# Kernel optimization log

Hardware: AMD Instinct MI355X
Metric: run time of the kernel (lower is better)

## Reference

```python
import jax, jax.numpy as jnp
import numpy as np

PARTIAL_DATA_THRESHOLD = 0.1  # threshold on squared NN distance (ChamferDistance returns squared dists)


def setup_inputs() -> dict:
    key = jax.random.key(0)
    k1, k2 = jax.random.split(key)
    scan_vertices = jax.random.normal(k1, (50000, 3), dtype=jnp.float32)      # N x 3
    template_vertices = jax.random.normal(k2, (6890, 3), dtype=jnp.float32)   # M x 3
    return {"scan_vertices": scan_vertices, "template_vertices": template_vertices}


def reference(scan_vertices, template_vertices):
    # Directional (template -> scan) Chamfer: for each template point, squared
    # distance to nearest scan point; then sum distances below threshold.
    # d2[m, n] = |t_m|^2 + |s_n|^2 - 2 t_m . s_n
    t_sq = jnp.sum(template_vertices * template_vertices, axis=-1)            # [M]
    s_sq = jnp.sum(scan_vertices * scan_vertices, axis=-1)                    # [N]
    cross = jnp.einsum('md,nd->mn', template_vertices, scan_vertices)         # [M, N]
    d2 = t_sq[:, None] + s_sq[None, :] - 2.0 * cross                          # [M, N]
    template2scan = jnp.min(d2, axis=1)                                       # [M]
    mask = template2scan < PARTIAL_DATA_THRESHOLD
    return jnp.sum(jnp.where(mask, template2scan, 0.0))
```

## Files before the change

### kernel.cpp

```cpp
#include <hip/hip_runtime.h>
#include <hip/hip_bf16.h>

#define BLK 256
#define WPB 4
#define TB 12
#define TSPLITS 18
#define SA 11
#define SSPLITS 144
#define FRTOT 1584
#define NSLOT (FRTOT * 32)
#define MFR 216
#define MPAD (MFR * 32)
#define THRESH 0.1f
#define KEY_MAX 0xFFFFFFFFu
#define ONE_BF ((unsigned short)0x3F80)

typedef __attribute__((ext_vector_type(8))) short short8;
typedef __attribute__((ext_vector_type(16))) float floatx16;

__device__ __forceinline__ unsigned short f2bf(float x) {
    unsigned u = __float_as_uint(x);
    unsigned r = u + 0x7FFFu + ((u >> 16) & 1u);
    return (unsigned short)(r >> 16);
}
__device__ __forceinline__ float bf2f(unsigned short h) {
    return __uint_as_float(((unsigned)h) << 16);
}

__device__ __forceinline__ unsigned f2key(float f) {
    unsigned b = __float_as_uint(f);
    return (b & 0x80000000u) ? ~b : (b | 0x80000000u);
}
__device__ __forceinline__ float key2f(unsigned k) {
    return __uint_as_float((k & 0x80000000u) ? (k & 0x7FFFFFFFu) : ~k);
}

__global__ __launch_bounds__(BLK) void pdl_prep(const float* __restrict__ scan,
                                                const float* __restrict__ tmpl,
                                                uint4* __restrict__ afrag,
                                                uint4* __restrict__ bfrag,
                                                unsigned* __restrict__ gmin,
                                                float* __restrict__ out,
                                                int N, int M) {
    const int n = blockIdx.x * BLK + threadIdx.x;
    if (n == 0) out[0] = 0.0f;

    if (n < MPAD) {
        gmin[n] = KEY_MAX;
        unsigned short q[16];
        if (n < M) {
            const float x = tmpl[3 * n + 0], y = tmpl[3 * n + 1], z = tmpl[3 * n + 2];
            const float t2 = fmaf(x, x, fmaf(y, y, z * z));
            const unsigned short xh = f2bf(x); const unsigned short xl = f2bf(x - bf2f(xh));
            const unsigned short yh = f2bf(y); const unsigned short yl = f2bf(y - bf2f(yh));
            const unsigned short zh = f2bf(z); const unsigned short zl = f2bf(z - bf2f(zh));
            const unsigned short wh = f2bf(t2); const unsigned short wl = f2bf(t2 - bf2f(wh));
            q[0] = xh; q[1] = xh; q[2] = xl; q[3] = xl;
            q[4] = yh; q[5] = yh; q[6] = yl; q[7] = yl;
            q[8] = zh; q[9] = zh; q[10] = zl; q[11] = zl;
            q[12] = wh; q[13] = wl;
            q[14] = ONE_BF; q[15] = ONE_BF;
        } else {
#pragma unroll
            for (int i = 0; i < 16; ++i) q[i] = 0;
            q[14] = ONE_BF; q[15] = ONE_BF;
        }
        const int g = n >> 5, c = n & 31;
        uint4 lo, hi;
        lo.x = (unsigned)q[0] | ((unsigned)q[1] << 16);
        lo.y = (unsigned)q[2] | ((unsigned)q[3] << 16);
        lo.z = (unsigned)q[4] | ((unsigned)q[5] << 16);
        lo.w = (unsigned)q[6] | ((unsigned)q[7] << 16);
        hi.x = (unsigned)q[8] | ((unsigned)q[9] << 16);
        hi.y = (unsigned)q[10] | ((unsigned)q[11] << 16);
        hi.z = (unsigned)q[12] | ((unsigned)q[13] << 16);
        hi.w = (unsigned)q[14] | ((unsigned)q[15] << 16);
        bfrag[(size_t)g * 64 + c] = lo;
        bfrag[(size_t)g * 64 + 32 + c] = hi;
    }

    if (n >= NSLOT) return;

    unsigned short k[16];
    if (n < N) {
        const float x = scan[3 * n + 0], y = scan[3 * n + 1], z = scan[3 * n + 2];
        const float s2 = fmaf(x, x, fmaf(y, y, z * z));
        const float cx = -2.0f * x, cy = -2.0f * y, cz = -2.0f * z;
        const unsigned short xh = f2bf(cx); const unsigned short xl = f2bf(cx - bf2f(xh));
        const unsigned short yh = f2bf(cy); const unsigned short yl = f2bf(cy - bf2f(yh));
        const unsigned short zh = f2bf(cz); const unsigned short zl = f2bf(cz - bf2f(zh));
        const unsigned short wh = f2bf(s2); const unsigned short wl = f2bf(s2 - bf2f(wh));
        k[0] = xh; k[1] = xl; k[2] = xh; k[3] = xl;
        k[4] = yh; k[5] = yl; k[6] = yh; k[7] = yl;
        k[8] = zh; k[9] = zl; k[10] = zh; k[11] = zl;
        k[12] = ONE_BF; k[13] = ONE_BF;
        k[14] = wh; k[15] = wl;
    } else {
#pragma unroll
        for (int i = 0; i < 16; ++i) k[i] = 0;
        k[12] = ONE_BF; k[13] = ONE_BF;
        k[14] = f2bf(1e30f); k[15] = 0;
    }

    const int g = n >> 5, c = n & 31;
    uint4 lo, hi;
    lo.x = (unsigned)k[0] | ((unsigned)k[1] << 16);
    lo.y = (unsigned)k[2] | ((unsigned)k[3] << 16);
    lo.z = (unsigned)k[4] | ((unsigned)k[5] << 16);
    lo.w = (unsigned)k[6] | ((unsigned)k[7] << 16);
    hi.x = (unsigned)k[8] | ((unsigned)k[9] << 16);
    hi.y = (unsigned)k[10] | ((unsigned)k[11] << 16);
    hi.z = (unsigned)k[12] | ((unsigned)k[13] << 16);
    hi.w = (unsigned)k[14] | ((unsigned)k[15] << 16);
    afrag[(size_t)g * 64 + c] = lo;
    afrag[(size_t)g * 64 + 32 + c] = hi;
}

__global__ __launch_bounds__(BLK, 3) void pdl_main(const uint4* __restrict__ afrag,
                                                   const uint4* __restrict__ bfrag,
                                                   unsigned* __restrict__ gmin) {
    const int tid = threadIdx.x;
    const int wave = tid >> 6, lane = tid & 63;
    const int tsplit = blockIdx.x;
    const int ssplit = blockIdx.y * WPB + wave;

    __shared__ unsigned lmin[TB * 32];
#pragma unroll 2
    for (int i = tid; i < TB * 32; i += BLK) lmin[i] = KEY_MAX;

    union U { uint4 u; short8 s; };

    const uint4* bb = bfrag + (size_t)(tsplit * TB) * 64 + lane;
    U B[TB];
#pragma unroll
    for (int j = 0; j < TB; ++j) B[j].u = bb[(size_t)j * 64];

    float mn[TB];
#pragma unroll
    for (int j = 0; j < TB; ++j) mn[j] = 3e30f;

    floatx16 zacc;
#pragma unroll
    for (int r = 0; r < 16; ++r) zacc[r] = 0.0f;

    __syncthreads();

    const uint4* ab = afrag + (size_t)(ssplit * SA) * 64 + lane;
    uint4 p = ab[0];
#pragma unroll 1
    for (int f = 0; f < SA; ++f) {
        U a; a.u = p;
        p = ab[(size_t)(f + 1) * 64];
#pragma unroll
        for (int j = 0; j < TB; ++j) {
            const floatx16 d =
                __builtin_amdgcn_mfma_f32_32x32x16_bf16(a.s, B[j].s, zacc, 0, 0, 0);
            const float t0 = fminf(fminf(d[0], d[1]), d[2]);
            const float t1 = fminf(fminf(d[3], d[4]), d[5]);
            const float t2 = fminf(fminf(d[6], d[7]), d[8]);
            const float t3 = fminf(fminf(d[9], d[10]), d[11]);
            const float t4 = fminf(fminf(d[12], d[13]), d[14]);
            const float u0 = fminf(fminf(t0, t1), t2);
            const float u1 = fminf(fminf(t3, t4), d[15]);
            mn[j] = fminf(fminf(u0, u1), mn[j]);
        }
    }

#pragma unroll
    for (int j = 0; j < TB; ++j) {
        const float o = __shfl_xor(mn[j], 32, 64);
        const float v = fminf(mn[j], o);
        if (lane < 32) atomicMin(&lmin[j * 32 + lane], f2key(v));
    }
    __syncthreads();

    const int mbase = tsplit * (TB * 32);
#pragma unroll 2
    for (int i = tid; i < TB * 32; i += BLK) atomicMin(&gmin[mbase + i], lmin[i]);
}

__global__ __launch_bounds__(BLK) void pdl_final(const unsigned* __restrict__ gmin,
                                                 float* __restrict__ out, int M) {
    const int m = blockIdx.x * BLK + threadIdx.x;
    float s = 0.0f;
    if (m < M) {
        const float v = key2f(gmin[m]);
        if (v < THRESH) s = v;
    }
#pragma unroll
    for (int off = 32; off > 0; off >>= 1) s += __shfl_down(s, off, 64);

    __shared__ float ls[BLK / 64];
    const int lane = threadIdx.x & 63;
    const int w = threadIdx.x >> 6;
    if (lane == 0) ls[w] = s;
    __syncthreads();
    if (threadIdx.x == 0) {
        float t = 0.0f;
#pragma unroll
        for (int i = 0; i < BLK / 64; ++i) t += ls[i];
        atomicAdd(out, t);
    }
}

extern "C" void kernel_launch(void* const* d_in, const int* in_sizes, int n_in,
                              void* d_out, int out_size, void* d_ws, size_t ws_size,
                              hipStream_t stream) {
    const float* scan = (const float*)d_in[0];
    const float* tmpl = (const float*)d_in[1];
    float* out = (float*)d_out;

    const int N = in_sizes[0] / 3;
    const int M = in_sizes[1] / 3;

    unsigned* gmin = (unsigned*)d_ws;
    uint4* afrag = (uint4*)((char*)d_ws + 65536);
    uint4* bfrag = (uint4*)((char*)d_ws + 65536 + (size_t)(FRTOT + 2) * 1024);

    pdl_prep<<<(NSLOT + BLK - 1) / BLK, BLK, 0, stream>>>(scan, tmpl, afrag, bfrag,
                                                          gmin, out, N, M);

    dim3 grid(TSPLITS, SSPLITS / WPB);
    pdl_main<<<grid, BLK, 0, stream>>>(afrag, bfrag, gmin);

    pdl_final<<<(M + BLK - 1) / BLK, BLK, 0, stream>>>(gmin, out, M);
}
```

Before: 73.03 us.

## Fuse fragment preparation into main kernel and replace global atomics with partial buffers

Removes the separate prep kernel: the main kernel now loads raw scan and template points and builds the split-bf16 MFMA fragments in registers, prefetching the next scan point each iteration. Global atomicMin into a shared min array is replaced by per-scan-group partial minima written to workspace, which the final kernel reduces over 36 groups. This saves a launch and the fragment round-trip through memory, at the cost of extra conversion ALU work inside the MFMA loop and a larger final reduction.

```diff
diff --git a/kernel.cpp b/kernel.cpp
--- a/kernel.cpp
+++ b/kernel.cpp
@@ -6,14 +6,11 @@
 #define TB 12
 #define TSPLITS 18
 #define SA 11
-#define SSPLITS 144
-#define FRTOT 1584
-#define NSLOT (FRTOT * 32)
-#define MFR 216
-#define MPAD (MFR * 32)
+#define SGROUPS 36
+#define COLS (TSPLITS * TB * 32)
 #define THRESH 0.1f
 #define KEY_MAX 0xFFFFFFFFu
-#define ONE_BF ((unsigned short)0x3F80)
+#define ONE2 0x3F803F80u
 
 typedef __attribute__((ext_vector_type(8))) short short8;
 typedef __attribute__((ext_vector_type(16))) float floatx16;
@@ -26,6 +23,11 @@
 __device__ __forceinline__ float bf2f(unsigned short h) {
     return __uint_as_float(((unsigned)h) << 16);
 }
+__device__ __forceinline__ unsigned packsplit(float v) {
+    const unsigned short h = f2bf(v);
+    const unsigned short l = f2bf(v - bf2f(h));
+    return (unsigned)h | ((unsigned)l << 16);
+}
 
 __device__ __forceinline__ unsigned f2key(float f) {
     unsigned b = __float_as_uint(f);
@@ -35,94 +37,52 @@
     return __uint_as_float((k & 0x80000000u) ? (k & 0x7FFFFFFFu) : ~k);
 }
 
-__global__ __launch_bounds__(BLK) void pdl_prep(const float* __restrict__ scan,
-                                                const float* __restrict__ tmpl,
-                                                uint4* __restrict__ afrag,
-                                                uint4* __restrict__ bfrag,
-                                                unsigned* __restrict__ gmin,
-                                                float* __restrict__ out,
-                                                int N, int M) {
-    const int n = blockIdx.x * BLK + threadIdx.x;
-    if (n == 0) out[0] = 0.0f;
-
-    if (n < MPAD) {
-        gmin[n] = KEY_MAX;
-        unsigned short q[16];
-        if (n < M) {
-            const float x = tmpl[3 * n + 0], y = tmpl[3 * n + 1], z = tmpl[3 * n + 2];
-            const float t2 = fmaf(x, x, fmaf(y, y, z * z));
-            const unsigned short xh = f2bf(x); const unsigned short xl = f2bf(x - bf2f(xh));
-            const unsigned short yh = f2bf(y); const unsigned short yl = f2bf(y - bf2f(yh));
-            const unsigned short zh = f2bf(z); const unsigned short zl = f2bf(z - bf2f(zh));
-            const unsigned short wh = f2bf(t2); const unsigned short wl = f2bf(t2 - bf2f(wh));
-            q[0] = xh; q[1] = xh; q[2] = xl; q[3] = xl;
-            q[4] = yh; q[5] = yh; q[6] = yl; q[7] = yl;
-            q[8] = zh; q[9] = zh; q[10] = zl; q[11] = zl;
-            q[12] = wh; q[13] = wl;
-            q[14] = ONE_BF; q[15] = ONE_BF;
-        } else {
-#pragma unroll
-            for (int i = 0; i < 16; ++i) q[i] = 0;
-            q[14] = ONE_BF; q[15] = ONE_BF;
-        }
-        const int g = n >> 5, c = n & 31;
-        uint4 lo, hi;
-        lo.x = (unsigned)q[0] | ((unsigned)q[1] << 16);
-        lo.y = (unsigned)q[2] | ((unsigned)q[3] << 16);
-        lo.z = (unsigned)q[4] | ((unsigned)q[5] << 16);
-        lo.w = (unsigned)q[6] | ((unsigned)q[7] << 16);
-        hi.x = (unsigned)q[8] | ((unsigned)q[9] << 16);
-        hi.y = (unsigned)q[10] | ((unsigned)q[11] << 16);
-        hi.z = (unsigned)q[12] | ((unsigned)q[13] << 16);
-        hi.w = (unsigned)q[14] | ((unsigned)q[15] << 16);
-        bfrag[(size_t)g * 64 + c] = lo;
-        bfrag[(size_t)g * 64 + 32 + c] = hi;
-    }
-
-    if (n >= NSLOT) return;
-
-    unsigned short k[16];
-    if (n < N) {
-        const float x = scan[3 * n + 0], y = scan[3 * n + 1], z = scan[3 * n + 2];
-        const float s2 = fmaf(x, x, fmaf(y, y, z * z));
-        const float cx = -2.0f * x, cy = -2.0f * y, cz = -2.0f * z;
-        const unsigned short xh = f2bf(cx); const unsigned short xl = f2bf(cx - bf2f(xh));
-        const unsigned short yh = f2bf(cy); const unsigned short yl = f2bf(cy - bf2f(yh));
-        const unsigned short zh = f2bf(cz); const unsigned short zl = f2bf(cz - bf2f(zh));
-        const unsigned short wh = f2bf(s2); const unsigned short wl = f2bf(s2 - bf2f(wh));
-        k[0] = xh; k[1] = xl; k[2] = xh; k[3] = xl;
-        k[4] = yh; k[5] = yl; k[6] = yh; k[7] = yl;
-        k[8] = zh; k[9] = zl; k[10] = zh; k[11] = zl;
-        k[12] = ONE_BF; k[13] = ONE_BF;
-        k[14] = wh; k[15] = wl;
-    } else {
-#pragma unroll
-        for (int i = 0; i < 16; ++i) k[i] = 0;
-        k[12] = ONE_BF; k[13] = ONE_BF;
-        k[14] = f2bf(1e30f); k[15] = 0;
-    }
-
-    const int g = n >> 5, c = n & 31;
-    uint4 lo, hi;
-    lo.x = (unsigned)k[0] | ((unsigned)k[1] << 16);
-    lo.y = (unsigned)k[2] | ((unsigned)k[3] << 16);
-    lo.z = (unsigned)k[4] | ((unsigned)k[5] << 16);
-    lo.w = (unsigned)k[6] | ((unsigned)k[7] << 16);
-    hi.x = (unsigned)k[8] | ((unsigned)k[9] << 16);
-    hi.y = (unsigned)k[10] | ((unsigned)k[11] << 16);
-    hi.z = (unsigned)k[12] | ((unsigned)k[13] << 16);
-    hi.w = (unsigned)k[14] | ((unsigned)k[15] << 16);
-    afrag[(size_t)g * 64 + c] = lo;
-    afrag[(size_t)g * 64 + 32 + c] = hi;
+__device__ __forceinline__ uint4 build_scan_frag(float x, float y, float z, bool hi) {
+    const float s2 = fmaf(x, x, fmaf(y, y, z * z));
+    const float c0 = -2.0f * (hi ? z : x);
+    const float c1 = hi ? s2 : (-2.0f * y);
+    const unsigned w01 = packsplit(c0);
+    const unsigned w23 = packsplit(c1);
+    uint4 u;
+    u.x = w01; u.y = w01;
+    u.z = hi ? ONE2 : w23;
+    u.w = w23;
+    return u;
 }
 
-__global__ __launch_bounds__(BLK, 3) void pdl_main(const uint4* __restrict__ afrag,
-                                                   const uint4* __restrict__ bfrag,
-                                                   unsigned* __restrict__ gmin) {
+__device__ __forceinline__ uint4 build_tmpl_frag(const float* __restrict__ tmpl,
+                                                 int c, bool hi) {
+    const float x = tmpl[3 * c + 0], y = tmpl[3 * c + 1], z = tmpl[3 * c + 2];
+    const float t2 = fmaf(x, x, fmaf(y, y, z * z));
+    const float a0 = hi ? z : x;
+    const float a1 = hi ? t2 : y;
+    const unsigned short h0 = f2bf(a0);
+    const unsigned short l0 = f2bf(a0 - bf2f(h0));
+    const unsigned short h1 = f2bf(a1);
+    const unsigned short l1 = f2bf(a1 - bf2f(h1));
+    uint4 u;
+    u.x = (unsigned)h0 | ((unsigned)h0 << 16);
+    u.y = (unsigned)l0 | ((unsigned)l0 << 16);
+    u.z = hi ? ((unsigned)h1 | ((unsigned)l1 << 16))
+             : ((unsigned)h1 | ((unsigned)h1 << 16));
+    u.w = hi ? ONE2
+             : ((unsigned)l1 | ((unsigned)l1 << 16));
+    return u;
+}
+
+__global__ __launch_bounds__(BLK, 3) void pdl_main(const float* __restrict__ scan,
+                                                   const float* __restrict__ tmpl,
+                                                   unsigned* __restrict__ partial,
+                                                   float* __restrict__ out,
+                                                   int N, int M) {
     const int tid = threadIdx.x;
     const int wave = tid >> 6, lane = tid & 63;
+    const bool hi = (lane >= 32);
     const int tsplit = blockIdx.x;
-    const int ssplit = blockIdx.y * WPB + wave;
+    const int sgroup = blockIdx.y;
+    const int ssplit = sgroup * WPB + wave;
+
+    if (tsplit == 0 && sgroup == 0 && tid == 0) out[0] = 0.0f;
 
     __shared__ unsigned lmin[TB * 32];
 #pragma unroll 2
@@ -130,10 +90,14 @@
 
     union U { uint4 u; short8 s; };
 
-    const uint4* bb = bfrag + (size_t)(tsplit * TB) * 64 + lane;
     U B[TB];
+    const int cbase = tsplit * (TB * 32) + (lane & 31);
 #pragma unroll
-    for (int j = 0; j < TB; ++j) B[j].u = bb[(size_t)j * 64];
+    for (int j = 0; j < TB; ++j) {
+        int c = cbase + j * 32;
+        if (c > M - 1) c = M - 1;
+        B[j].u = build_tmpl_frag(tmpl, c, hi);
+    }
 
     float mn[TB];
 #pragma unroll
@@ -143,14 +107,16 @@
 #pragma unroll
     for (int r = 0; r < 16; ++r) zacc[r] = 0.0f;
 
-    __syncthreads();
-
-    const uint4* ab = afrag + (size_t)(ssplit * SA) * 64 + lane;
-    uint4 p = ab[0];
+    const int nbase = ssplit * (SA * 32) + (lane & 31);
+    int n0 = nbase; if (n0 > N - 1) n0 = N - 1;
+    float x = scan[3 * n0 + 0], y = scan[3 * n0 + 1], z = scan[3 * n0 + 2];
 #pragma unroll 1
     for (int f = 0; f < SA; ++f) {
-        U a; a.u = p;
-        p = ab[(size_t)(f + 1) * 64];
+        int n1 = nbase + (f + 1) * 32; if (n1 > N - 1) n1 = N - 1;
+        const float nx = scan[3 * n1 + 0];
+        const float ny = scan[3 * n1 + 1];
+        const float nz = scan[3 * n1 + 2];
+        U a; a.u = build_scan_frag(x, y, z, hi);
 #pragma unroll
         for (int j = 0; j < TB; ++j) {
             const floatx16 d =
@@ -164,7 +130,10 @@
             const float u1 = fminf(fminf(t3, t4), d[15]);
             mn[j] = fminf(fminf(u0, u1), mn[j]);
         }
+        x = nx; y = ny; z = nz;
     }
+
+    __syncthreads();
 
 #pragma unroll
     for (int j = 0; j < TB; ++j) {
@@ -174,17 +143,21 @@
     }
     __syncthreads();
 
-    const int mbase = tsplit * (TB * 32);
+    const size_t base = (size_t)sgroup * COLS + (size_t)tsplit * (TB * 32);
 #pragma unroll 2
-    for (int i = tid; i < TB * 32; i += BLK) atomicMin(&gmin[mbase + i], lmin[i]);
+    for (int i = tid; i < TB * 32; i += BLK) partial[base + i] = lmin[i];
 }
 
-__global__ __launch_bounds__(BLK) void pdl_final(const unsigned* __restrict__ gmin,
+__global__ __launch_bounds__(BLK) void pdl_final(const unsigned* __restrict__ partial,
                                                  float* __restrict__ out, int M) {
     const int m = blockIdx.x * BLK + threadIdx.x;
     float s = 0.0f;
     if (m < M) {
-        const float v = key2f(gmin[m]);
+        unsigned k = KEY_MAX;
+#pragma unroll 4
+        for (int g = 0; g < SGROUPS; ++g)
+            k = min(k, partial[(size_t)g * COLS + m]);
+        const float v = key2f(k);
         if (v < THRESH) s = v;
     }
 #pragma unroll
@@ -213,15 +186,10 @@
     const int N = in_sizes[0] / 3;
     const int M = in_sizes[1] / 3;
 
-    unsigned* gmin = (unsigned*)d_ws;
-    uint4* afrag = (uint4*)((char*)d_ws + 65536);
-    uint4* bfrag = (uint4*)((char*)d_ws + 65536 + (size_t)(FRTOT + 2) * 1024);
+    unsigned* partial = (unsigned*)d_ws;
 
-    pdl_prep<<<(NSLOT + BLK - 1) / BLK, BLK, 0, stream>>>(scan, tmpl, afrag, bfrag,
-                                                          gmin, out, N, M);
+    dim3 grid(TSPLITS, SGROUPS);
+    pdl_main<<<grid, BLK, 0, stream>>>(scan, tmpl, partial, out, N, M);
 
-    dim3 grid(TSPLITS, SSPLITS / WPB);
-    pdl_main<<<grid, BLK, 0, stream>>>(afrag, bfrag, gmin);
-
-    pdl_final<<<(M + BLK - 1) / BLK, BLK, 0, stream>>>(gmin, out, M);
+    pdl_final<<<(M + BLK - 1) / BLK, BLK, 0, stream>>>(partial, out, M);
 }
```

Measured after the change: 75.81 us. 1.04x slower.
